# Kernel optimization log

Hardware: AMD Instinct MI355X
Metric: run time of the kernel (lower is better)

## Reference

```python
import jax, jax.numpy as jnp
import numpy as np

NEG_SLOPE = 0.2
EPS = 0.0  # default eps, non-trainable buffer
N_NODES = 50000
N_EDGES = 400000
D = 512  # state_dim


def setup_inputs() -> dict:
    key = jax.random.key(0)
    ks = jax.random.split(key, 8)
    x = jax.random.normal(ks[0], (N_NODES, D), dtype=jnp.float32)
    row = jax.random.randint(ks[1], (N_EDGES,), 0, N_NODES)
    col = jax.random.randint(ks[2], (N_EDGES,), 0, N_NODES)
    # remove_self_loops: guarantee no self loops at data-gen time (static shapes)
    col = jnp.where(row == col, (col + 1) % N_NODES, col)
    edge_index = jnp.stack([row, col], axis=0)  # [2, E]
    condition = jax.random.normal(ks[3], (1, 256), dtype=jnp.float32)
    scale = 1.0 / np.sqrt(256.0)
    Wk = jax.random.normal(ks[4], (256, 2 * D), dtype=jnp.float32) * scale
    W1 = jax.random.normal(ks[5], (D, 2 * D), dtype=jnp.float32) / np.sqrt(D)
    b1 = jnp.zeros((2 * D,), dtype=jnp.float32)
    W2 = jax.random.normal(ks[6], (2 * D, D), dtype=jnp.float32) / np.sqrt(2 * D)
    b2 = jnp.zeros((D,), dtype=jnp.float32)
    return {"x": x, "edge_index": edge_index, "condition": condition,
            "Wk": Wk, "W1": W1, "b1": b1, "W2": W2, "b2": b2}


def reference(x, edge_index, condition, Wk, W1, b1, W2, b2):
    row, col = edge_index[0], edge_index[1]
    key = condition @ Wk                      # [1, 2D]
    ki, kj = key[0, :D], key[0, D:]           # x_i pairs with first half, x_j with second
    x_i = x[col]                              # [E, D]
    # alpha = (cat([x_i, x_j]) * key).sum(-1) without materializing the concat
    alpha = x_i @ ki + x[row] @ kj            # [E]
    alpha = jnp.where(alpha >= 0, alpha, NEG_SLOPE * alpha)  # leaky_relu
    alpha = jax.nn.sigmoid(alpha)
    agg = jax.ops.segment_sum(x_i * alpha[:, None], row, num_segments=x.shape[0])
    out = (1.0 + EPS) * x + agg
    out = jax.nn.relu(out @ W1 + b1) @ W2 + b2  # h_Theta MLP
    return out
```

## Files before the change

### kernel.cpp

```cpp
#include <hip/hip_runtime.h>

#define D 512
#define H1 1024
#define NNODES 50000
#define NEDGES 400000
#define MPAD 50176
#define NEG_SLOPE 0.2f
#define SCAN_BLOCKS 196

typedef __attribute__((ext_vector_type(8))) short bf16x8;
typedef __attribute__((ext_vector_type(8))) unsigned short u16x8;
typedef __attribute__((ext_vector_type(4))) float f32x4;


__device__ __forceinline__ unsigned short f2bf(float f) {
  unsigned int u = __float_as_uint(f);
  unsigned int r = u + 0x7FFFu + ((u >> 16) & 1u);
  return (unsigned short)(r >> 16);
}
__device__ __forceinline__ float bf2f(unsigned short h) {
  return __uint_as_float((unsigned int)h << 16);
}

__device__ __forceinline__ void gl_lds16(const void* g, void* l) {
  __builtin_amdgcn_global_load_lds(
      (const __attribute__((address_space(1))) void*)g,
      (__attribute__((address_space(3))) void*)l, 16, 0, 0);
}

__global__ void key_kernel(const float* __restrict__ cond, const float* __restrict__ Wk,
                           float* __restrict__ key) {
  int j = blockIdx.x * blockDim.x + threadIdx.x;
  if (j >= 2 * D) return;
  float s = 0.f;
#pragma unroll 8
  for (int i = 0; i < 256; ++i) s += cond[i] * Wk[i * (2 * D) + j];
  key[j] = s;
}

__global__ void nodedot_kernel(const float* __restrict__ x, const float* __restrict__ key,
                               float* __restrict__ nki, float* __restrict__ nkj,
                               unsigned short* __restrict__ xb) {
  int wid = (blockIdx.x * blockDim.x + threadIdx.x) >> 6;
  int lane = threadIdx.x & 63;
  if (wid >= NNODES) return;
  const float4* xr = (const float4*)(x + (size_t)wid * D);
  float4 p0 = xr[2 * lane], p1 = xr[2 * lane + 1];
  const float4* kia = (const float4*)key;
  const float4* kja = (const float4*)(key + D);
  float4 q0 = kia[2 * lane], q1 = kia[2 * lane + 1];
  float4 r0 = kja[2 * lane], r1 = kja[2 * lane + 1];
  float a = p0.x * q0.x + p0.y * q0.y + p0.z * q0.z + p0.w * q0.w +
            p1.x * q1.x + p1.y * q1.y + p1.z * q1.z + p1.w * q1.w;
  float b = p0.x * r0.x + p0.y * r0.y + p0.z * r0.z + p0.w * r0.w +
            p1.x * r1.x + p1.y * r1.y + p1.z * r1.z + p1.w * r1.w;
  u16x8 h;
  h[0] = f2bf(p0.x); h[1] = f2bf(p0.y); h[2] = f2bf(p0.z); h[3] = f2bf(p0.w);
  h[4] = f2bf(p1.x); h[5] = f2bf(p1.y); h[6] = f2bf(p1.z); h[7] = f2bf(p1.w);
  *(u16x8*)(xb + (size_t)wid * D + 8 * lane) = h;
#pragma unroll
  for (int off = 32; off > 0; off >>= 1) {
    a += __shfl_xor(a, off);
    b += __shfl_xor(b, off);
  }
  if (lane == 0) { nki[wid] = a; nkj[wid] = b; }
}

__global__ void convw_kernel(const float* __restrict__ W1, const float* __restrict__ W2,
                             unsigned short* __restrict__ W1t, unsigned short* __restrict__ W2t) {
  int idx = blockIdx.x * blockDim.x + threadIdx.x;
  if (idx >= D * H1) return;
  {
    int k = idx / H1, n = idx % H1;
    size_t a = (((size_t)(n >> 7) * (D >> 3) + (k >> 3)) << 10) + ((n & 127) << 3) + (k & 7);
    W1t[a] = f2bf(W1[idx]);
  }
  {
    int k = idx / D, n = idx % D;
    size_t a = (((size_t)(n >> 7) * (H1 >> 3) + (k >> 3)) << 10) + ((n & 127) << 3) + (k & 7);
    W2t[a] = f2bf(W2[idx]);
  }
}

__global__ void zero_deg_kernel(int* __restrict__ deg) {
  int i = blockIdx.x * blockDim.x + threadIdx.x;
  if (i < NNODES) deg[i] = 0;
}

__global__ void hist_kernel(const int* __restrict__ row, int* __restrict__ deg) {
  int e = blockIdx.x * blockDim.x + threadIdx.x;
  if (e < NEDGES) atomicAdd(&deg[row[e]], 1);
}

__global__ void scan1_kernel(const int* __restrict__ deg, int* __restrict__ rowptr,
                             int* __restrict__ blktot) {
  __shared__ int s[256];
  int tid = threadIdx.x;
  int i = blockIdx.x * 256 + tid;
  int v = (i < NNODES) ? deg[i] : 0;
  s[tid] = v;
  __syncthreads();
#pragma unroll
  for (int off = 1; off < 256; off <<= 1) {
    int t = (tid >= off) ? s[tid - off] : 0;
    __syncthreads();
    s[tid] += t;
    __syncthreads();
  }
  if (i < NNODES) rowptr[i] = s[tid] - v;
  if (tid == 255) blktot[blockIdx.x] = s[255];
}

__global__ void scan2_kernel(int* __restrict__ blktot, int* __restrict__ blkoff) {
  __shared__ int s[256];
  int tid = threadIdx.x;
  int v = (tid < SCAN_BLOCKS) ? blktot[tid] : 0;
  s[tid] = v;
  __syncthreads();
#pragma unroll
  for (int off = 1; off < 256; off <<= 1) {
    int t = (tid >= off) ? s[tid - off] : 0;
    __syncthreads();
    s[tid] += t;
    __syncthreads();
  }
  if (tid < SCAN_BLOCKS) blkoff[tid] = s[tid] - v;
}

__global__ void scan3_kernel(int* __restrict__ rowptr, const int* __restrict__ blkoff,
                             int* __restrict__ cursor) {
  int i = blockIdx.x * blockDim.x + threadIdx.x;
  if (i < NNODES) {
    int v = rowptr[i] + blkoff[blockIdx.x];
    rowptr[i] = v;
    cursor[i] = v;
  }
  if (i == 0) rowptr[NNODES] = NEDGES;
}

__global__ void fill_kernel(const int* __restrict__ row, const int* __restrict__ col,
                            const float* __restrict__ nki, const float* __restrict__ nkj,
                            int* __restrict__ cursor, int* __restrict__ scol,
                            float* __restrict__ salpha) {
  int e = blockIdx.x * blockDim.x + threadIdx.x;
  if (e >= NEDGES) return;
  int r = row[e], c = col[e];
  float a = nki[c] + nkj[r];
  a = (a >= 0.f) ? a : NEG_SLOPE * a;
  float al = 1.f / (1.f + expf(-a));
  int pos = atomicAdd(&cursor[r], 1);
  scol[pos] = c;
  salpha[pos] = al;
}

__global__ __launch_bounds__(256) void agg_kernel(
    const unsigned short* __restrict__ xb, const int* __restrict__ rowptr,
    const int* __restrict__ scol, const float* __restrict__ salpha,
    unsigned short* __restrict__ Pb) {
  int n = (blockIdx.x * blockDim.x + threadIdx.x) >> 6;
  int lane = threadIdx.x & 63;
  if (n >= NNODES) return;
  int beg = rowptr[n], end = rowptr[n + 1];
  u16x8 self = *(const u16x8*)(xb + (size_t)n * D + 8 * lane);
  float sa[8], sb[8];
#pragma unroll
  for (int q = 0; q < 8; ++q) { sa[q] = bf2f(self[q]); sb[q] = 0.f; }
  int e = beg;
  for (; e + 1 < end; e += 2) {
    int c0 = scol[e], c1 = scol[e + 1];
    float al0 = salpha[e], al1 = salpha[e + 1];
    u16x8 w0 = *(const u16x8*)(xb + (size_t)c0 * D + 8 * lane);
    u16x8 w1 = *(const u16x8*)(xb + (size_t)c1 * D + 8 * lane);
#pragma unroll
    for (int q = 0; q < 8; ++q) {
      sa[q] += al0 * bf2f(w0[q]);
      sb[q] += al1 * bf2f(w1[q]);
    }
  }
  if (e < end) {
    int c0 = scol[e];
    float al0 = salpha[e];
    u16x8 w0 = *(const u16x8*)(xb + (size_t)c0 * D + 8 * lane);
#pragma unroll
    for (int q = 0; q < 8; ++q) sa[q] += al0 * bf2f(w0[q]);
  }
  u16x8 h;
#pragma unroll
  for (int q = 0; q < 8; ++q) h[q] = f2bf(sa[q] + sb[q]);
  *(u16x8*)(Pb + (((size_t)(n >> 7) * (D >> 3) + lane) << 10) + ((n & 127) << 3)) = h;
}

template <int K, bool RELU_OUT_BF16>
__global__ __launch_bounds__(512, 2) void gemm_kernel(
    const unsigned short* __restrict__ Ag, const unsigned short* __restrict__ Bt,
    const float* __restrict__ bias, void* __restrict__ Cptr, int M_valid, int N) {
  constexpr int KC = K >> 3;
  constexpr int NT = K >> 6;
  __shared__ unsigned short As[2 * 2 * 8 * 128 * 8];
  __shared__ unsigned short Bs[2 * 2 * 8 * 128 * 8];

  const int G = gridDim.x * gridDim.y;
  const int orig = blockIdx.y * gridDim.x + blockIdx.x;
  const int wg = (orig & 7) * (G >> 3) + (orig >> 3);
  const int bx = wg % gridDim.x;
  const int by = wg / gridDim.x;

  const int tid = threadIdx.x;
  const int lane = tid & 63;
  const int wave = tid >> 6;
  const int wr = wave >> 2;
  const int wc = wave & 3;
  const int fr = lane & 15;
  const int kq = lane >> 4;

  f32x4 acc[8][4];
#pragma unroll
  for (int i = 0; i < 8; ++i)
#pragma unroll
    for (int j = 0; j < 4; ++j)
#pragma unroll
      for (int r = 0; r < 4; ++r) acc[i][j][r] = 0.f;

  auto stage = [&](int b, int t) {
#pragma unroll
    for (int ss = 0; ss < 4; ++ss) {
      const int s = wave * 4 + ss;
      const int rb = s >> 4, kc = (s >> 1) & 7, half = s & 1;
      const int kca = t * 8 + kc;
      gl_lds16(Ag + (((size_t)(by * 2 + rb) * KC + kca) << 10) + (half * 64 + lane) * 8,
               &As[((b * 2 + rb) * 8 + kc) * 1024 + half * 512]);
      gl_lds16(Bt + (((size_t)(bx * 2 + rb) * KC + kca) << 10) + (half * 64 + lane) * 8,
               &Bs[((b * 2 + rb) * 8 + kc) * 1024 + half * 512]);
    }
  };

  const int rbB = wc >> 1;
  const int rowB = (wc & 1) * 64;

  stage(0, 0);
  stage(1, 1);

  for (int t = 0; t < NT - 1; ++t) {
    const int cur = t & 1;
    asm volatile("s_waitcnt vmcnt(8)" ::: "memory");
    __builtin_amdgcn_s_barrier();
    __builtin_amdgcn_sched_barrier(0);

    {
      const int kc = kq;
      bf16x8 af[8], bfv[4];
#pragma unroll
      for (int i = 0; i < 8; ++i)
        af[i] = *(const bf16x8*)&As[((cur * 2 + wr) * 8 + kc) * 1024 + (i * 16 + fr) * 8];
#pragma unroll
      for (int j = 0; j < 4; ++j)
        bfv[j] = *(const bf16x8*)&Bs[((cur * 2 + rbB) * 8 + kc) * 1024 + (rowB + j * 16 + fr) * 8];
      __builtin_amdgcn_s_setprio(1);
#pragma unroll
      for (int i = 0; i < 8; ++i)
#pragma unroll
        for (int j = 0; j < 4; ++j)
          acc[i][j] = __builtin_amdgcn_mfma_f32_16x16x32_bf16(af[i], bfv[j], acc[i][j], 0, 0, 0);
      __builtin_amdgcn_s_setprio(0);
    }

    bf16x8 af1[8], bf1[4];
    {
      const int kc = 4 + kq;
#pragma unroll
      for (int i = 0; i < 8; ++i)
        af1[i] = *(const bf16x8*)&As[((cur * 2 + wr) * 8 + kc) * 1024 + (i * 16 + fr) * 8];
#pragma unroll
      for (int j = 0; j < 4; ++j)
        bf1[j] = *(const bf16x8*)&Bs[((cur * 2 + rbB) * 8 + kc) * 1024 + (rowB + j * 16 + fr) * 8];
    }
    asm volatile("s_waitcnt lgkmcnt(0)" ::: "memory");
    __builtin_amdgcn_sched_barrier(0);
    __builtin_amdgcn_s_barrier();
    if (t + 2 < NT) stage(cur, t + 2);
    __builtin_amdgcn_sched_barrier(0);
    __builtin_amdgcn_s_setprio(1);
#pragma unroll
    for (int i = 0; i < 8; ++i)
#pragma unroll
      for (int j = 0; j < 4; ++j)
        acc[i][j] = __builtin_amdgcn_mfma_f32_16x16x32_bf16(af1[i], bf1[j], acc[i][j], 0, 0, 0);
    __builtin_amdgcn_s_setprio(0);
  }

  {
    const int cur = (NT - 1) & 1;
    asm volatile("s_waitcnt vmcnt(0)" ::: "memory");
    __builtin_amdgcn_s_barrier();
    __builtin_amdgcn_sched_barrier(0);
#pragma unroll
    for (int h = 0; h < 2; ++h) {
      const int kc = h * 4 + kq;
      bf16x8 af[8], bfv[4];
#pragma unroll
      for (int i = 0; i < 8; ++i)
        af[i] = *(const bf16x8*)&As[((cur * 2 + wr) * 8 + kc) * 1024 + (i * 16 + fr) * 8];
#pragma unroll
      for (int j = 0; j < 4; ++j)
        bfv[j] = *(const bf16x8*)&Bs[((cur * 2 + rbB) * 8 + kc) * 1024 + (rowB + j * 16 + fr) * 8];
      __builtin_amdgcn_s_setprio(1);
#pragma unroll
      for (int i = 0; i < 8; ++i)
#pragma unroll
        for (int j = 0; j < 4; ++j)
          acc[i][j] = __builtin_amdgcn_mfma_f32_16x16x32_bf16(af[i], bfv[j], acc[i][j], 0, 0, 0);
      __builtin_amdgcn_s_setprio(0);
    }
  }

  const int rg = kq * 4;
#pragma unroll
  for (int j = 0; j < 4; ++j) {
    const int gn = bx * 256 + wc * 64 + j * 16 + fr;
    const float bv = bias[gn];
#pragma unroll
    for (int i = 0; i < 8; ++i) {
#pragma unroll
      for (int r = 0; r < 4; ++r) {
        const int lrow = wr * 128 + i * 16 + rg + r;
        const int gm = by * 256 + lrow;
        float v = acc[i][j][r] + bv;
        if constexpr (RELU_OUT_BF16) {
          v = fmaxf(v, 0.f);
          size_t a = (((size_t)(gm >> 7) * (N >> 3) + (gn >> 3)) << 10) + ((gm & 127) << 3) + (gn & 7);
          ((unsigned short*)Cptr)[a] = f2bf(v);
        } else {
          if (gm < M_valid) ((float*)Cptr)[(size_t)gm * N + gn] = v;
        }
      }
    }
  }
}

extern "C" void kernel_launch(void* const* d_in, const int* in_sizes, int n_in,
                              void* d_out, int out_size, void* d_ws, size_t ws_size,
                              hipStream_t stream) {
  const float* x    = (const float*)d_in[0];
  const int*   ei   = (const int*)d_in[1];
  const float* cond = (const float*)d_in[2];
  const float* Wk   = (const float*)d_in[3];
  const float* W1   = (const float*)d_in[4];
  const float* b1   = (const float*)d_in[5];
  const float* W2   = (const float*)d_in[6];
  const float* b2   = (const float*)d_in[7];
  float* out = (float*)d_out;

  char* ws = (char*)d_ws;
  size_t off = 0;
  auto alloc = [&](size_t b) { size_t p = off; off += (b + 255) & ~(size_t)255; return p; };
  float* key = (float*)(ws + alloc(2 * D * sizeof(float)));
  float* nki = (float*)(ws + alloc(NNODES * sizeof(float)));
  float* nkj = (float*)(ws + alloc(NNODES * sizeof(float)));
  int* deg    = (int*)(ws + alloc(NNODES * sizeof(int)));
  int* rowptr = (int*)(ws + alloc((NNODES + 1) * sizeof(int)));
  int* cursor = (int*)(ws + alloc(NNODES * sizeof(int)));
  int* blktot = (int*)(ws + alloc(SCAN_BLOCKS * sizeof(int)));
  int* blkoff = (int*)(ws + alloc(SCAN_BLOCKS * sizeof(int)));
  int* scol      = (int*)(ws + alloc(NEDGES * sizeof(int)));
  float* salpha  = (float*)(ws + alloc(NEDGES * sizeof(float)));
  unsigned short* xb  = (unsigned short*)(ws + alloc((size_t)NNODES * D * 2));
  unsigned short* W1t = (unsigned short*)(ws + alloc((size_t)H1 * D * 2));
  unsigned short* W2t = (unsigned short*)(ws + alloc((size_t)D * H1 * 2));
  unsigned short* Pb  = (unsigned short*)(ws + alloc((size_t)MPAD * D * 2));
  unsigned short* Hb  = (unsigned short*)(ws + alloc((size_t)MPAD * H1 * 2));

  const int* row = ei;
  const int* col = ei + NEDGES;

  key_kernel<<<dim3((2 * D + 255) / 256), dim3(256), 0, stream>>>(cond, Wk, key);
  nodedot_kernel<<<dim3(NNODES * 64 / 256), dim3(256), 0, stream>>>(x, key, nki, nkj, xb);
  convw_kernel<<<dim3(D * H1 / 256), dim3(256), 0, stream>>>(W1, W2, W1t, W2t);

  zero_deg_kernel<<<dim3(SCAN_BLOCKS), dim3(256), 0, stream>>>(deg);
  hist_kernel<<<dim3((NEDGES + 255) / 256), dim3(256), 0, stream>>>(row, deg);
  scan1_kernel<<<dim3(SCAN_BLOCKS), dim3(256), 0, stream>>>(deg, rowptr, blktot);
  scan2_kernel<<<dim3(1), dim3(256), 0, stream>>>(blktot, blkoff);
  scan3_kernel<<<dim3(SCAN_BLOCKS), dim3(256), 0, stream>>>(rowptr, blkoff, cursor);
  fill_kernel<<<dim3((NEDGES + 255) / 256), dim3(256), 0, stream>>>(row, col, nki, nkj,
                                                                    cursor, scol, salpha);
  agg_kernel<<<dim3(NNODES * 64 / 256 + 1), dim3(256), 0, stream>>>(xb, rowptr, scol, salpha, Pb);

  gemm_kernel<512, true><<<dim3(H1 / 256, MPAD / 256), dim3(512), 0, stream>>>(
      Pb, W1t, b1, Hb, NNODES, H1);
  gemm_kernel<1024, false><<<dim3(D / 256, MPAD / 256), dim3(512), 0, stream>>>(
      Hb, W2t, b2, out, NNODES, D);
}
```

Before: 371.3 us.

## Restructure GEMM main loop into half-K staged phases with finer-grained prefetch

Splits each K-tile's global-to-LDS staging into two halves and issues them at different points in the iteration. Each K step now runs as four phases of 4x4 MFMAs with their own LDS reads, waitcnt and barrier, instead of two 8x4 blocks. The goal is to spread memory traffic more evenly and overlap loads with compute while holding fewer A fragments in registers. In exchange it adds barriers per iteration and relies on hand-tuned vmcnt counts that must match the number of outstanding loads.

```diff
diff --git a/kernel.cpp b/kernel.cpp
--- a/kernel.cpp
+++ b/kernel.cpp
@@ -212,6 +212,8 @@
   const int wc = wave & 3;
   const int fr = lane & 15;
   const int kq = lane >> 4;
+  const int rbB = wc >> 1;
+  const int rowB = (wc & 1) * 64;
 
   f32x4 acc[8][4];
 #pragma unroll
@@ -221,97 +223,72 @@
 #pragma unroll
       for (int r = 0; r < 4; ++r) acc[i][j][r] = 0.f;
 
-  auto stage = [&](int b, int t) {
-#pragma unroll
-    for (int ss = 0; ss < 4; ++ss) {
-      const int s = wave * 4 + ss;
-      const int rb = s >> 4, kc = (s >> 1) & 7, half = s & 1;
+  auto stage_half = [&](int b, int t, int kk) {
+#pragma unroll
+    for (int ss = 0; ss < 2; ++ss) {
+      const int s = wave * 2 + ss;
+      const int rb = s >> 3;
+      const int kc = kk * 4 + ((s >> 1) & 3);
+      const int h64 = s & 1;
       const int kca = t * 8 + kc;
-      gl_lds16(Ag + (((size_t)(by * 2 + rb) * KC + kca) << 10) + (half * 64 + lane) * 8,
-               &As[((b * 2 + rb) * 8 + kc) * 1024 + half * 512]);
-      gl_lds16(Bt + (((size_t)(bx * 2 + rb) * KC + kca) << 10) + (half * 64 + lane) * 8,
-               &Bs[((b * 2 + rb) * 8 + kc) * 1024 + half * 512]);
+      gl_lds16(Ag + (((size_t)(by * 2 + rb) * KC + kca) << 10) + (h64 * 64 + lane) * 8,
+               &As[((b * 2 + rb) * 8 + kc) * 1024 + h64 * 512]);
+      gl_lds16(Bt + (((size_t)(bx * 2 + rb) * KC + kca) << 10) + (h64 * 64 + lane) * 8,
+               &Bs[((b * 2 + rb) * 8 + kc) * 1024 + h64 * 512]);
     }
   };
 
-  const int rbB = wc >> 1;
-  const int rowB = (wc & 1) * 64;
-
-  stage(0, 0);
-  stage(1, 1);
-
-  for (int t = 0; t < NT - 1; ++t) {
-    const int cur = t & 1;
-    asm volatile("s_waitcnt vmcnt(8)" ::: "memory");
+  stage_half(0, 0, 0);
+  stage_half(0, 0, 1);
+  stage_half(1, 1, 0);
+  __builtin_amdgcn_sched_barrier(0);
+
+#define PHASE(BUF, IH, KK, READB)                                                       \
+  {                                                                                     \
+    const int kc_ = (KK) * 4 + kq;                                                      \
+    bf16x8 af[4];                                                                       \
+    _Pragma("unroll") for (int i = 0; i < 4; ++i)                                       \
+        af[i] = *(const bf16x8*)&As[(((BUF) * 2 + wr) * 8 + kc_) * 1024 +               \
+                                    ((IH) * 64 + i * 16 + fr) * 8];                     \
+    if (READB) {                                                                        \
+      _Pragma("unroll") for (int j = 0; j < 4; ++j)                                     \
+          bfv[j] = *(const bf16x8*)&Bs[(((BUF) * 2 + rbB) * 8 + kc_) * 1024 +           \
+                                       (rowB + j * 16 + fr) * 8];                       \
+    }                                                                                   \
+    asm volatile("s_waitcnt lgkmcnt(0)" ::: "memory");                                  \
+    __builtin_amdgcn_sched_barrier(0);                                                  \
+    __builtin_amdgcn_s_setprio(1);                                                      \
+    _Pragma("unroll") for (int i = 0; i < 4; ++i)                                       \
+        _Pragma("unroll") for (int j = 0; j < 4; ++j)                                   \
+            acc[(IH) * 4 + i][j] = __builtin_amdgcn_mfma_f32_16x16x32_bf16(             \
+                af[i], bfv[j], acc[(IH) * 4 + i][j], 0, 0, 0);                          \
+    __builtin_amdgcn_s_setprio(0);                                                      \
+    __builtin_amdgcn_s_barrier();                                                       \
+  }
+
+#pragma unroll
+  for (int t = 0; t < NT; ++t) {
+    const int buf = t & 1;
+    bf16x8 bfv[4];
+    __builtin_amdgcn_sched_barrier(0);
+    if (t + 1 < NT) stage_half(buf ^ 1, t + 1, 1);
+    __builtin_amdgcn_sched_barrier(0);
+    if (t < NT - 1) { asm volatile("s_waitcnt vmcnt(12)" ::: "memory"); }
+    else            { asm volatile("s_waitcnt vmcnt(4)" ::: "memory"); }
     __builtin_amdgcn_s_barrier();
+    PHASE(buf, 0, 0, true)
+    PHASE(buf, 1, 0, false)
     __builtin_amdgcn_sched_barrier(0);
-
-    {
-      const int kc = kq;
-      bf16x8 af[8], bfv[4];
-#pragma unroll
-      for (int i = 0; i < 8; ++i)
-        af[i] = *(const bf16x8*)&As[((cur * 2 + wr) * 8 + kc) * 1024 + (i * 16 + fr) * 8];
-#pragma unroll
-      for (int j = 0; j < 4; ++j)
-        bfv[j] = *(const bf16x8*)&Bs[((cur * 2 + rbB) * 8 + kc) * 1024 + (rowB + j * 16 + fr) * 8];
-      __builtin_amdgcn_s_setprio(1);
-#pragma unroll
-      for (int i = 0; i < 8; ++i)
-#pragma unroll
-        for (int j = 0; j < 4; ++j)
-          acc[i][j] = __builtin_amdgcn_mfma_f32_16x16x32_bf16(af[i], bfv[j], acc[i][j], 0, 0, 0);
-      __builtin_amdgcn_s_setprio(0);
-    }
-
-    bf16x8 af1[8], bf1[4];
-    {
-      const int kc = 4 + kq;
-#pragma unroll
-      for (int i = 0; i < 8; ++i)
-        af1[i] = *(const bf16x8*)&As[((cur * 2 + wr) * 8 + kc) * 1024 + (i * 16 + fr) * 8];
-#pragma unroll
-      for (int j = 0; j < 4; ++j)
-        bf1[j] = *(const bf16x8*)&Bs[((cur * 2 + rbB) * 8 + kc) * 1024 + (rowB + j * 16 + fr) * 8];
-    }
-    asm volatile("s_waitcnt lgkmcnt(0)" ::: "memory");
+    if (t + 2 < NT) stage_half(buf, t + 2, 0);
     __builtin_amdgcn_sched_barrier(0);
+    if (t < NT - 2)      { asm volatile("s_waitcnt vmcnt(12)" ::: "memory"); }
+    else if (t == NT - 2){ asm volatile("s_waitcnt vmcnt(8)" ::: "memory"); }
+    else                 { asm volatile("s_waitcnt vmcnt(0)" ::: "memory"); }
     __builtin_amdgcn_s_barrier();
-    if (t + 2 < NT) stage(cur, t + 2);
-    __builtin_amdgcn_sched_barrier(0);
-    __builtin_amdgcn_s_setprio(1);
-#pragma unroll
-    for (int i = 0; i < 8; ++i)
-#pragma unroll
-      for (int j = 0; j < 4; ++j)
-        acc[i][j] = __builtin_amdgcn_mfma_f32_16x16x32_bf16(af1[i], bf1[j], acc[i][j], 0, 0, 0);
-    __builtin_amdgcn_s_setprio(0);
-  }
-
-  {
-    const int cur = (NT - 1) & 1;
-    asm volatile("s_waitcnt vmcnt(0)" ::: "memory");
-    __builtin_amdgcn_s_barrier();
-    __builtin_amdgcn_sched_barrier(0);
-#pragma unroll
-    for (int h = 0; h < 2; ++h) {
-      const int kc = h * 4 + kq;
-      bf16x8 af[8], bfv[4];
-#pragma unroll
-      for (int i = 0; i < 8; ++i)
-        af[i] = *(const bf16x8*)&As[((cur * 2 + wr) * 8 + kc) * 1024 + (i * 16 + fr) * 8];
-#pragma unroll
-      for (int j = 0; j < 4; ++j)
-        bfv[j] = *(const bf16x8*)&Bs[((cur * 2 + rbB) * 8 + kc) * 1024 + (rowB + j * 16 + fr) * 8];
-      __builtin_amdgcn_s_setprio(1);
-#pragma unroll
-      for (int i = 0; i < 8; ++i)
-#pragma unroll
-        for (int j = 0; j < 4; ++j)
-          acc[i][j] = __builtin_amdgcn_mfma_f32_16x16x32_bf16(af[i], bfv[j], acc[i][j], 0, 0, 0);
-      __builtin_amdgcn_s_setprio(0);
-    }
-  }
+    PHASE(buf, 0, 1, true)
+    PHASE(buf, 1, 1, false)
+  }
+#undef PHASE
 
   const int rg = kq * 4;
 #pragma unroll
```

After: 407.4 us. 1.1x slower.
